# Performance work log

Measured on AMD Instinct MI355X. Metric: run time of the kernel, lower is better.

The kernel has to match this reference:

```python
import jax, jax.numpy as jnp
import numpy as np

BS = 4
EMBED = 256
HEADS = 8
LEVELS = 4
POINTS = 4
HD = EMBED // HEADS  # 32
SHAPES = np.array([[96, 96], [48, 48], [24, 24], [12, 12]], dtype=np.int64)
LQ = int((SHAPES[:, 0] * SHAPES[:, 1]).sum())  # 12240


def _offset_bias():
    # faithful to MSDeformableAttention._reset_parameters grid init
    thetas = np.arange(HEADS, dtype=np.float32) * (2.0 * np.pi / HEADS)
    g = np.stack([np.cos(thetas), np.sin(thetas)], -1)
    g = g / np.abs(g).max(-1, keepdims=True)
    g = np.tile(g.reshape(HEADS, 1, 1, 2), (1, LEVELS, POINTS, 1))
    g = g * np.arange(1, POINTS + 1, dtype=np.float32).reshape(1, 1, -1, 1)
    return jnp.asarray(g.reshape(-1), dtype=jnp.float32)


def setup_inputs() -> dict:
    key = jax.random.key(0)
    ks = jax.random.split(key, 8)
    tp = HEADS * LEVELS * POINTS
    d = {}
    d["query"] = jax.random.normal(ks[0], (BS, LQ, EMBED), jnp.float32)
    d["reference_points"] = jax.random.uniform(ks[1], (BS, LQ, LEVELS, 2), jnp.float32)
    d["value"] = jax.random.normal(ks[2], (BS, LQ, EMBED), jnp.float32)
    d["value_spatial_shapes"] = SHAPES  # static numpy, int
    d["W_off"] = jax.random.normal(ks[3], (EMBED, tp * 2), jnp.float32) * 0.01
    d["b_off"] = _offset_bias()
    d["W_attn"] = jax.random.normal(ks[4], (EMBED, tp), jnp.float32) * 0.02
    d["b_attn"] = jnp.zeros((tp,), jnp.float32)
    d["W_val"] = jax.random.normal(ks[5], (EMBED, EMBED), jnp.float32) * (1.0 / np.sqrt(EMBED).astype(np.float32))
    d["b_val"] = jnp.zeros((EMBED,), jnp.float32)
    d["W_out"] = jax.random.normal(ks[6], (EMBED, EMBED), jnp.float32) * (1.0 / np.sqrt(EMBED).astype(np.float32))
    d["b_out"] = jnp.zeros((EMBED,), jnp.float32)
    return d


def _bilinear_sample(img, grid):
    # img: [B,H,W,C]; grid: [B,Q,P,2] in [-1,1] (x,y)
    # matches F.grid_sample(mode='bilinear', padding_mode='zeros', align_corners=False)
    B, H, W, C = img.shape
    gx = (grid[..., 0] + 1.0) * (W * 0.5) - 0.5
    gy = (grid[..., 1] + 1.0) * (H * 0.5) - 0.5
    x0 = jnp.floor(gx)
    y0 = jnp.floor(gy)
    wx = gx - x0
    wy = gy - y0
    x0i = x0.astype(jnp.int32)
    y0i = y0.astype(jnp.int32)
    x1i = x0i + 1
    y1i = y0i + 1
    flat = img.reshape(B, H * W, C)

    def corner(xi, yi, w):
        valid = (xi >= 0) & (xi < W) & (yi >= 0) & (yi < H)
        idx = jnp.clip(yi, 0, H - 1) * W + jnp.clip(xi, 0, W - 1)
        v = jnp.take_along_axis(flat, idx.reshape(B, -1, 1), axis=1)
        v = v.reshape(idx.shape + (C,))
        return v * (w * valid)[..., None]

    return (corner(x0i, y0i, (1.0 - wx) * (1.0 - wy))
            + corner(x1i, y0i, wx * (1.0 - wy))
            + corner(x0i, y1i, (1.0 - wx) * wy)
            + corner(x1i, y1i, wx * wy))


def reference(query, reference_points, value, value_spatial_shapes,
              W_off, b_off, W_attn, b_attn, W_val, b_val, W_out, b_out):
    shapes = np.asarray(value_spatial_shapes)  # static [L,2] (H,W)
    bs, Lq, _ = query.shape
    v = (value @ W_val + b_val).reshape(bs, -1, HEADS, HD)  # [bs,Lv,H,hd]
    off = (query @ W_off + b_off).reshape(bs, Lq, HEADS, LEVELS, POINTS, 2)
    aw = jax.nn.softmax((query @ W_attn + b_attn).reshape(bs, Lq, HEADS, LEVELS * POINTS), axis=-1)
    aw = aw.reshape(bs, Lq, HEADS, LEVELS, POINTS)
    # normalizer is (W,H) per level
    norm = jnp.asarray(shapes[:, ::-1].copy(), jnp.float32).reshape(1, 1, 1, LEVELS, 1, 2)
    loc = reference_points[:, :, None, :, None, :] + off / norm
    grids = 2.0 * loc - 1.0  # [bs,Lq,H,L,P,2]

    acc = jnp.zeros((bs * HEADS, Lq, HD), query.dtype)
    start = 0
    for lvl in range(LEVELS):
        h, w = int(shapes[lvl, 0]), int(shapes[lvl, 1])
        v_l = v[:, start:start + h * w].reshape(bs, h, w, HEADS, HD)
        v_l = v_l.transpose(0, 3, 1, 2, 4).reshape(bs * HEADS, h, w, HD)
        g_l = grids[:, :, :, lvl].transpose(0, 2, 1, 3, 4).reshape(bs * HEADS, Lq, POINTS, 2)
        s_l = _bilinear_sample(v_l, g_l)  # [bs*H, Lq, P, hd]
        w_l = aw[:, :, :, lvl].transpose(0, 2, 1, 3).reshape(bs * HEADS, Lq, POINTS)
        acc = acc + jnp.einsum('bqpc,bqp->bqc', s_l, w_l)
        start += h * w

    out = acc.reshape(bs, HEADS, Lq, HD).transpose(0, 2, 1, 3).reshape(bs, Lq, EMBED)
    return out @ W_out + b_out
```

## Files before the change

kernel.cpp:

```cpp
#include <hip/hip_runtime.h>
#include <hip/hip_bf16.h>

static constexpr int BS     = 4;
static constexpr int EMBED  = 256;
static constexpr int HEADS  = 8;
static constexpr int LEVELS = 4;
static constexpr int POINTS = 4;
static constexpr int HD     = 32;
static constexpr int LQ     = 12240;
static constexpr int NROW   = BS * LQ;
static constexpr int LVL_W[4]  = {96, 48, 24, 12};
static constexpr int LVL_H[4]  = {96, 48, 24, 12};
static constexpr int LVL_ST[4] = {0, 9216, 11520, 12096};

typedef __attribute__((ext_vector_type(8))) short short8;
typedef __attribute__((ext_vector_type(4))) float f32x4;
typedef _Float16 h2 __attribute__((ext_vector_type(2)));

__device__ __forceinline__ unsigned short f2bf(float f) {
    unsigned int u = __float_as_uint(f);
    unsigned int r = (u + 0x7FFFu + ((u >> 16) & 1u)) >> 16;
    return (unsigned short)r;
}

__device__ __forceinline__ unsigned int pkh(float a, float b) {
    const unsigned int ua = __builtin_bit_cast(unsigned short, (_Float16)a);
    const unsigned int ub = __builtin_bit_cast(unsigned short, (_Float16)b);
    return ua | (ub << 16);
}

__device__ __forceinline__ float dot2(float acc, unsigned int v, unsigned int w) {
#if __has_builtin(__builtin_amdgcn_fdot2)
    return __builtin_amdgcn_fdot2(__builtin_bit_cast(h2, v),
                                  __builtin_bit_cast(h2, w), acc, false);
#else
    asm("v_dot2_f32_f16 %0, %1, %2, %0" : "+v"(acc) : "v"(v), "v"(w));
    return acc;
#endif
}

__global__ __launch_bounds__(256) void prep_weights(
    const float* __restrict__ W_off, const float* __restrict__ W_attn,
    const float* __restrict__ W_val, const float* __restrict__ W_out,
    unsigned short* __restrict__ WT_oa, unsigned short* __restrict__ WT_val,
    unsigned short* __restrict__ WT_out)
{
    const int gid = blockIdx.x * 256 + threadIdx.x;
    const int k = gid & 255;
    const int n = gid >> 8;
    if (n < 384) {
        const float v = (n < 256) ? W_off[k * 256 + n] : W_attn[k * 128 + (n - 256)];
        WT_oa[n * 256 + k] = f2bf(v);
    } else if (n < 640) {
        const int nn = n - 384;
        WT_val[nn * 256 + k] = f2bf(W_val[k * 256 + nn]);
    } else {
        const int nn = n - 640;
        WT_out[nn * 256 + k] = f2bf(W_out[k * 256 + nn]);
    }
}

template <int NCH, bool A_BF16, int OMODE>
__global__ __launch_bounds__(256, 3) void gemm_persist(
    const void* __restrict__ Av, const unsigned short* __restrict__ Wt,
    const float* __restrict__ bias0, const float* __restrict__ bias1, int nsplit,
    void* __restrict__ Cv)
{
    constexpr int K = 256;
    __shared__ __align__(16) unsigned short Af[64][264];
    __shared__ __align__(16) unsigned short Bs[128][40];

    const int tid = threadIdx.x;
    const int m0 = blockIdx.x * 64;
    const int w  = tid >> 6;
    const int l  = tid & 63;
    const int lm = l & 15;
    const int lq = l >> 4;

    const int sr = tid >> 2;
    const int kg = (tid & 3) * 8;

    if (A_BF16) {
        const unsigned short* A = (const unsigned short*)Av;
        #pragma unroll
        for (int k0 = 0; k0 < K; k0 += 32)
            *(short8*)&Af[sr][k0 + kg] = *(const short8*)&A[(size_t)(m0 + sr) * K + k0 + kg];
    } else {
        const float* A = (const float*)Av;
        #pragma unroll
        for (int k0 = 0; k0 < K; k0 += 32) {
            const float* ap = &A[(size_t)(m0 + sr) * K + k0 + kg];
            const float4 a0 = *(const float4*)ap;
            const float4 a1 = *(const float4*)(ap + 4);
            uint4 pk;
            pk.x = (unsigned int)f2bf(a0.x) | ((unsigned int)f2bf(a0.y) << 16);
            pk.y = (unsigned int)f2bf(a0.z) | ((unsigned int)f2bf(a0.w) << 16);
            pk.z = (unsigned int)f2bf(a1.x) | ((unsigned int)f2bf(a1.y) << 16);
            pk.w = (unsigned int)f2bf(a1.z) | ((unsigned int)f2bf(a1.w) << 16);
            *(uint4*)&Af[sr][k0 + kg] = pk;
        }
    }

    short8 pb[2];
    auto gloadB = [&](int n0, int k0) {
        #pragma unroll
        for (int i = 0; i < 2; ++i) {
            const int slot = tid + i * 256;
            const int n  = slot >> 2;
            const int kk = (slot & 3) * 8;
            pb[i] = *(const short8*)&Wt[(size_t)(n0 + n) * K + k0 + kk];
        }
    };
    gloadB(0, 0);
    __syncthreads();

    #pragma unroll
    for (int ch = 0; ch < NCH; ++ch) {
        const int n0 = ch * 128;
        f32x4 acc[4][2];
        #pragma unroll
        for (int rg = 0; rg < 4; ++rg) {
            acc[rg][0] = (f32x4){0.f, 0.f, 0.f, 0.f};
            acc[rg][1] = (f32x4){0.f, 0.f, 0.f, 0.f};
        }

        #pragma unroll 2
        for (int k0 = 0; k0 < K; k0 += 32) {
            #pragma unroll
            for (int i = 0; i < 2; ++i) {
                const int slot = tid + i * 256;
                const int n  = slot >> 2;
                const int kk = (slot & 3) * 8;
                *(short8*)&Bs[n][kk] = pb[i];
            }
            __syncthreads();

            if (k0 + 32 < K)       gloadB(n0, k0 + 32);
            else if (ch + 1 < NCH) gloadB(n0 + 128, 0);

            short8 af[4];
            #pragma unroll
            for (int rg = 0; rg < 4; ++rg)
                af[rg] = *(const short8*)&Af[rg * 16 + lm][k0 + lq * 8];
            #pragma unroll
            for (int nt = 0; nt < 2; ++nt) {
                const short8 bf = *(const short8*)&Bs[(w * 2 + nt) * 16 + lm][lq * 8];
                #pragma unroll
                for (int rg = 0; rg < 4; ++rg)
                    acc[rg][nt] = __builtin_amdgcn_mfma_f32_16x16x32_bf16(af[rg], bf, acc[rg][nt], 0, 0, 0);
            }
            __syncthreads();
        }

        #pragma unroll
        for (int nt = 0; nt < 2; ++nt) {
            const int col = n0 + (w * 2 + nt) * 16 + lm;
            const float b = (col < nsplit) ? bias0[col] : bias1[col - nsplit];
            #pragma unroll
            for (int rg = 0; rg < 4; ++rg)
                #pragma unroll
                for (int r = 0; r < 4; ++r) {
                    const int row = m0 + rg * 16 + lq * 4 + r;
                    const float v = acc[rg][nt][r] + b;
                    if (OMODE == 0)
                        ((unsigned short*)Cv)[(size_t)row * 256 + col] =
                            __builtin_bit_cast(unsigned short, (_Float16)v);
                    else if (OMODE == 1)
                        ((float*)Cv)[(size_t)row * 384 + col] = v;
                    else
                        ((float*)Cv)[(size_t)row * 256 + col] = v;
                }
        }
    }
}

__global__ __launch_bounds__(256, 4) void sample_kernel(
    const unsigned short* __restrict__ V,
    const float* __restrict__ OA,
    const float* __restrict__ refp,
    unsigned short* __restrict__ ACC)
{
    __shared__ __align__(16) unsigned int pr_o[512][4];
    __shared__ __align__(16) unsigned int pr_w[512][2];

    const int tid = threadIdx.x;

    const unsigned bx = blockIdx.x;
    const int xcd  = bx & 7;
    const int slot = bx >> 3;
    const int batch = xcd >> 1;
    const int wb   = slot * 2 + (xcd & 1);
    const int row0 = batch * LQ + wb * 4;

    {
        float4* dstb = (float4*)pr_o;
        const float4* src = (const float4*)(OA + (size_t)row0 * 384);
        {
            const int i = tid, rr = i / 96, ww = i % 96;
            dstb[rr * 96 + (ww ^ ((ww >> 3) & 7))] = src[i];
        }
        if (tid < 128) {
            const int i = tid + 256, rr = i / 96, ww = i % 96;
            dstb[rr * 96 + (ww ^ ((ww >> 3) & 7))] = src[i];
        }
        __syncthreads();

        const int g = tid & 31;
        const int r = g >> 3;
        const int h = g & 7;
        const int L = tid >> 5;
        const float* stg = (const float*)pr_o + r * 384;

        auto swzf4 = [](int f4) { return f4 ^ ((f4 >> 3) & 7); };

        const int f4l0 = 64 + ((h * 16 + L) >> 2);
        const int f4l1 = 64 + ((h * 16 + L + 8) >> 2);
        const float lg0 = stg[swzf4(f4l0) * 4 + (L & 3)];
        const float lg1 = stg[swzf4(f4l1) * 4 + (L & 3)];

        float* smax = (float*)pr_w;
        float* ssum = smax + 264;
        smax[L * 33 + g] = fmaxf(lg0, lg1);
        __syncthreads();
        float m = smax[g];
        #pragma unroll
        for (int k = 1; k < 8; ++k) m = fmaxf(m, smax[k * 33 + g]);
        const float e0 = __expf(lg0 - m);
        const float e1 = __expf(lg1 - m);
        ssum[L * 33 + g] = e0 + e1;
        __syncthreads();
        float sden = ssum[g];
        #pragma unroll
        for (int k = 1; k < 8; ++k) sden += ssum[k * 33 + g];
        const float inv = 1.0f / sden;

        uint4 ostash[2];
        uint2 wstash[2];
        int   sidx[2];
        #pragma unroll
        for (int ss = 0; ss < 2; ++ss) {
            const int lp  = L + ss * 8;
            const int s   = lp * 32 + g;
            const int lvl = lp >> 2;
            const int Wl = LVL_W[lvl], Hl = LVL_H[lvl], st = LVL_ST[lvl];

            const int f4c = h * 8 + (lp >> 1);
            const float2 oxy = *(const float2*)&stg[swzf4(f4c) * 4 + (lp & 1) * 2];
            const float2 rxy = *(const float2*)&refp[(size_t)(row0 + r) * 8 + lvl * 2];
            const float wgt = (ss ? e1 : e0) * inv;

            const float gx = (rxy.x + oxy.x / (float)Wl) * (float)Wl - 0.5f;
            const float gy = (rxy.y + oxy.y / (float)Hl) * (float)Hl - 0.5f;

            const float fx = floorf(gx), fy = floorf(gy);
            const float wx = gx - fx,    wy = gy - fy;
            const int x0 = (int)fx, y0 = (int)fy;
            const int x1 = x0 + 1,  y1 = y0 + 1;

            const bool bx0 = ((unsigned)x0 < (unsigned)Wl);
            const bool bx1 = ((unsigned)x1 < (unsigned)Wl);
            const bool by0 = ((unsigned)y0 < (unsigned)Hl);
            const bool by1 = ((unsigned)y1 < (unsigned)Hl);
            const float w00 = (bx0 && by0) ? (1.f - wx) * (1.f - wy) * wgt : 0.f;
            const float w10 = (bx1 && by0) ? wx * (1.f - wy) * wgt : 0.f;
            const float w01 = (bx0 && by1) ? (1.f - wx) * wy * wgt : 0.f;
            const float w11 = (bx1 && by1) ? wx * wy * wgt : 0.f;

            const int cx0 = min(max(x0, 0), Wl - 1);
            const int cx1 = min(max(x1, 0), Wl - 1);
            const int cy0 = min(max(y0, 0), Hl - 1);
            const int cy1 = min(max(y1, 0), Hl - 1);

            uint4 o;
            o.x = (unsigned int)(st + cy0 * Wl + cx0) * 512u;
            o.y = (unsigned int)(st + cy0 * Wl + cx1) * 512u;
            o.z = (unsigned int)(st + cy1 * Wl + cx0) * 512u;
            o.w = (unsigned int)(st + cy1 * Wl + cx1) * 512u;
            ostash[ss] = o;
            wstash[ss] = make_uint2(pkh(w00, w10), pkh(w01, w11));
            sidx[ss] = s;
        }
        __syncthreads();
        *(uint4*)&pr_o[sidx[0]][0] = ostash[0];
        *(uint4*)&pr_o[sidx[1]][0] = ostash[1];
        *(uint2*)&pr_w[sidx[0]][0] = wstash[0];
        *(uint2*)&pr_w[sidx[1]][0] = wstash[1];
    }
    __syncthreads();

    const int w    = tid >> 6;
    const int l    = tid & 63;
    const int half = l >> 5;
    const int head = (l >> 2) & 7;
    const int c16  = (l & 3) * 16;

    const int row  = __builtin_amdgcn_readfirstlane(row0 + w);
    const char* vrow = (const char*)V + (size_t)batch * ((size_t)LQ * 512);
    const unsigned int lane_byte = (unsigned int)(head * 64 + c16);
    const int sid0 = half * 256 + w * 8 + head;

    constexpr unsigned SEL_LO = 0x01000504u;
    constexpr unsigned SEL_HI = 0x03020706u;

    uint4 ofs[4];
    uint2 wpk[4];
    uint4 dat[3][4];
    float acc[8];
    #pragma unroll
    for (int i = 0; i < 8; ++i) acc[i] = 0.f;

    auto ldpr = [&](int j, int sl) {
        ofs[sl] = *(const uint4*)&pr_o[sid0 + j * 32][0];
        wpk[sl] = *(const uint2*)&pr_w[sid0 + j * 32][0];
    };
    auto ldglb = [&](int osl, int dsl) {
        const uint4 o = ofs[osl];
        dat[dsl][0] = *(const uint4*)(vrow + (lane_byte + o.x));
        dat[dsl][1] = *(const uint4*)(vrow + (lane_byte + o.y));
        dat[dsl][2] = *(const uint4*)(vrow + (lane_byte + o.z));
        dat[dsl][3] = *(const uint4*)(vrow + (lane_byte + o.w));
    };
    auto cpair = [&](const uint4& d0, const uint4& d1, unsigned wp) {
        acc[0] = dot2(acc[0], __builtin_amdgcn_perm(d0.x, d1.x, SEL_LO), wp);
        acc[1] = dot2(acc[1], __builtin_amdgcn_perm(d0.x, d1.x, SEL_HI), wp);
        acc[2] = dot2(acc[2], __builtin_amdgcn_perm(d0.y, d1.y, SEL_LO), wp);
        acc[3] = dot2(acc[3], __builtin_amdgcn_perm(d0.y, d1.y, SEL_HI), wp);
        acc[4] = dot2(acc[4], __builtin_amdgcn_perm(d0.z, d1.z, SEL_LO), wp);
        acc[5] = dot2(acc[5], __builtin_amdgcn_perm(d0.z, d1.z, SEL_HI), wp);
        acc[6] = dot2(acc[6], __builtin_amdgcn_perm(d0.w, d1.w, SEL_LO), wp);
        acc[7] = dot2(acc[7], __builtin_amdgcn_perm(d0.w, d1.w, SEL_HI), wp);
    };
    auto consume = [&](int dsl, int wsl) {
        cpair(dat[dsl][0], dat[dsl][1], wpk[wsl].x);
        cpair(dat[dsl][2], dat[dsl][3], wpk[wsl].y);
    };

    ldpr(0, 0); ldpr(1, 1); ldpr(2, 2);
    ldglb(0, 0); ldglb(1, 1);
    #pragma unroll
    for (int j = 0; j < 8; ++j) {
        if (j + 2 < 8) ldglb((j + 2) & 3, (j + 2) % 3);
        if (j + 3 < 8) ldpr(j + 3, (j + 3) & 3);
        consume(j % 3, j & 3);
    }

    #pragma unroll
    for (int i = 0; i < 8; ++i) acc[i] += __shfl_xor(acc[i], 32);

    if (half == 0) {
        uint4 o;
        o.x = (unsigned int)f2bf(acc[0]) | ((unsigned int)f2bf(acc[1]) << 16);
        o.y = (unsigned int)f2bf(acc[2]) | ((unsigned int)f2bf(acc[3]) << 16);
        o.z = (unsigned int)f2bf(acc[4]) | ((unsigned int)f2bf(acc[5]) << 16);
        o.w = (unsigned int)f2bf(acc[6]) | ((unsigned int)f2bf(acc[7]) << 16);
        *(uint4*)((char*)(ACC + (size_t)row * EMBED) + head * 64 + c16) = o;
    }
}

extern "C" void kernel_launch(void* const* d_in, const int* in_sizes, int n_in,
                              void* d_out, int out_size, void* d_ws, size_t ws_size,
                              hipStream_t stream) {
    const float* query  = (const float*)d_in[0];
    const float* refp   = (const float*)d_in[1];
    const float* value  = (const float*)d_in[2];
    const float* W_off  = (const float*)d_in[4];
    const float* b_off  = (const float*)d_in[5];
    const float* W_attn = (const float*)d_in[6];
    const float* b_attn = (const float*)d_in[7];
    const float* W_val  = (const float*)d_in[8];
    const float* b_val  = (const float*)d_in[9];
    const float* W_out  = (const float*)d_in[10];
    const float* b_out  = (const float*)d_in[11];
    float* out = (float*)d_out;

    unsigned short* WT_oa  = (unsigned short*)d_ws;
    unsigned short* WT_val = WT_oa  + 384 * 256;
    unsigned short* WT_out = WT_val + 256 * 256;
    unsigned short* V      = WT_out + 256 * 256;
    float*          OA     = (float*)(V + (size_t)NROW * EMBED);
    unsigned short* ACCb   = (unsigned short*)(OA + (size_t)NROW * 384);

    dim3 blk(256);

    prep_weights<<<896, blk, 0, stream>>>(W_off, W_attn, W_val, W_out,
                                          WT_oa, WT_val, WT_out);
    gemm_persist<2, false, 0><<<NROW / 64, blk, 0, stream>>>(
        value, WT_val, b_val, b_val, 256, V);
    gemm_persist<3, false, 1><<<NROW / 64, blk, 0, stream>>>(
        query, WT_oa, b_off, b_attn, 256, OA);
    sample_kernel<<<NROW / 4, blk, 0, stream>>>(V, OA, refp, ACCb);
    gemm_persist<2, true, 2><<<NROW / 64, blk, 0, stream>>>(
        ACCb, WT_out, b_out, b_out, 256, out);
}
```

Baseline: 320.1 us.

## Pre-convert inputs to bf16, use LDS-free direct-load GEMMs, tune sampler waits

A fused prep kernel now converts the weights and also the value and query activations to bf16 in one pass. The shared-memory-tiled GEMM is replaced by a direct-from-global MFMA GEMM over 32-row tiles, with no LDS or barriers. In the sampler, the LDS swizzle additionally XORs in the row index, and gathers use inline-asm loads with explicit vmcnt waits and sched barriers. Occupancy hints are relaxed. The trade-off is an extra activation round-trip through memory and more redundant global reads of A and W in the GEMMs.

```diff
diff --git a/kernel.cpp b/kernel.cpp
--- a/kernel.cpp
+++ b/kernel.cpp
@@ -39,117 +39,85 @@
 #endif
 }
 
-__global__ __launch_bounds__(256) void prep_weights(
+__global__ __launch_bounds__(256) void prep_all(
     const float* __restrict__ W_off, const float* __restrict__ W_attn,
     const float* __restrict__ W_val, const float* __restrict__ W_out,
+    const float* __restrict__ value, const float* __restrict__ query,
     unsigned short* __restrict__ WT_oa, unsigned short* __restrict__ WT_val,
-    unsigned short* __restrict__ WT_out)
+    unsigned short* __restrict__ WT_out,
+    unsigned short* __restrict__ Vb, unsigned short* __restrict__ Qb)
 {
-    const int gid = blockIdx.x * 256 + threadIdx.x;
-    const int k = gid & 255;
-    const int n = gid >> 8;
-    if (n < 384) {
-        const float v = (n < 256) ? W_off[k * 256 + n] : W_attn[k * 128 + (n - 256)];
-        WT_oa[n * 256 + k] = f2bf(v);
-    } else if (n < 640) {
-        const int nn = n - 384;
-        WT_val[nn * 256 + k] = f2bf(W_val[k * 256 + nn]);
-    } else {
-        const int nn = n - 640;
-        WT_out[nn * 256 + k] = f2bf(W_out[k * 256 + nn]);
-    }
-}
-
-template <int NCH, bool A_BF16, int OMODE>
-__global__ __launch_bounds__(256, 3) void gemm_persist(
-    const void* __restrict__ Av, const unsigned short* __restrict__ Wt,
+    const int bx = blockIdx.x;
+    const int tid = threadIdx.x;
+    if (bx < 896) {
+        const int gid = bx * 256 + tid;
+        const int k = gid & 255;
+        const int n = gid >> 8;
+        if (n < 384) {
+            const float v = (n < 256) ? W_off[k * 256 + n] : W_attn[k * 128 + (n - 256)];
+            WT_oa[n * 256 + k] = f2bf(v);
+        } else if (n < 640) {
+            const int nn = n - 384;
+            WT_val[nn * 256 + k] = f2bf(W_val[k * 256 + nn]);
+        } else {
+            const int nn = n - 640;
+            WT_out[nn * 256 + k] = f2bf(W_out[k * 256 + nn]);
+        }
+        return;
+    }
+    constexpr size_t NE = (size_t)NROW * 256;
+    const size_t i = ((size_t)(bx - 896) * 256 + tid) * 8;
+    const bool isV = (i < NE);
+    const float* src = isV ? value : query;
+    unsigned short* dst = isV ? Vb : Qb;
+    const size_t off = isV ? i : i - NE;
+    const float4 a0 = *(const float4*)&src[off];
+    const float4 a1 = *(const float4*)&src[off + 4];
+    uint4 pk;
+    pk.x = (unsigned int)f2bf(a0.x) | ((unsigned int)f2bf(a0.y) << 16);
+    pk.y = (unsigned int)f2bf(a0.z) | ((unsigned int)f2bf(a0.w) << 16);
+    pk.z = (unsigned int)f2bf(a1.x) | ((unsigned int)f2bf(a1.y) << 16);
+    pk.w = (unsigned int)f2bf(a1.z) | ((unsigned int)f2bf(a1.w) << 16);
+    *(uint4*)&dst[off] = pk;
+}
+
+template <int NCH, int OMODE>
+__global__ __launch_bounds__(256) void gemm_direct(
+    const unsigned short* __restrict__ A,
+    const unsigned short* __restrict__ Wt,
     const float* __restrict__ bias0, const float* __restrict__ bias1, int nsplit,
     void* __restrict__ Cv)
 {
-    constexpr int K = 256;
-    __shared__ __align__(16) unsigned short Af[64][264];
-    __shared__ __align__(16) unsigned short Bs[128][40];
-
     const int tid = threadIdx.x;
-    const int m0 = blockIdx.x * 64;
+    const int m0 = blockIdx.x * 32;
     const int w  = tid >> 6;
     const int l  = tid & 63;
     const int lm = l & 15;
     const int lq = l >> 4;
 
-    const int sr = tid >> 2;
-    const int kg = (tid & 3) * 8;
-
-    if (A_BF16) {
-        const unsigned short* A = (const unsigned short*)Av;
-        #pragma unroll
-        for (int k0 = 0; k0 < K; k0 += 32)
-            *(short8*)&Af[sr][k0 + kg] = *(const short8*)&A[(size_t)(m0 + sr) * K + k0 + kg];
-    } else {
-        const float* A = (const float*)Av;
-        #pragma unroll
-        for (int k0 = 0; k0 < K; k0 += 32) {
-            const float* ap = &A[(size_t)(m0 + sr) * K + k0 + kg];
-            const float4 a0 = *(const float4*)ap;
-            const float4 a1 = *(const float4*)(ap + 4);
-            uint4 pk;
-            pk.x = (unsigned int)f2bf(a0.x) | ((unsigned int)f2bf(a0.y) << 16);
-            pk.y = (unsigned int)f2bf(a0.z) | ((unsigned int)f2bf(a0.w) << 16);
-            pk.z = (unsigned int)f2bf(a1.x) | ((unsigned int)f2bf(a1.y) << 16);
-            pk.w = (unsigned int)f2bf(a1.z) | ((unsigned int)f2bf(a1.w) << 16);
-            *(uint4*)&Af[sr][k0 + kg] = pk;
-        }
-    }
-
-    short8 pb[2];
-    auto gloadB = [&](int n0, int k0) {
-        #pragma unroll
-        for (int i = 0; i < 2; ++i) {
-            const int slot = tid + i * 256;
-            const int n  = slot >> 2;
-            const int kk = (slot & 3) * 8;
-            pb[i] = *(const short8*)&Wt[(size_t)(n0 + n) * K + k0 + kk];
-        }
-    };
-    gloadB(0, 0);
-    __syncthreads();
+    const unsigned short* arow0 = &A[(size_t)(m0 + lm) * 256 + lq * 8];
+    const unsigned short* arow1 = arow0 + 16 * 256;
 
     #pragma unroll
     for (int ch = 0; ch < NCH; ++ch) {
         const int n0 = ch * 128;
-        f32x4 acc[4][2];
-        #pragma unroll
-        for (int rg = 0; rg < 4; ++rg) {
-            acc[rg][0] = (f32x4){0.f, 0.f, 0.f, 0.f};
-            acc[rg][1] = (f32x4){0.f, 0.f, 0.f, 0.f};
-        }
-
-        #pragma unroll 2
-        for (int k0 = 0; k0 < K; k0 += 32) {
-            #pragma unroll
-            for (int i = 0; i < 2; ++i) {
-                const int slot = tid + i * 256;
-                const int n  = slot >> 2;
-                const int kk = (slot & 3) * 8;
-                *(short8*)&Bs[n][kk] = pb[i];
-            }
-            __syncthreads();
-
-            if (k0 + 32 < K)       gloadB(n0, k0 + 32);
-            else if (ch + 1 < NCH) gloadB(n0 + 128, 0);
-
-            short8 af[4];
-            #pragma unroll
-            for (int rg = 0; rg < 4; ++rg)
-                af[rg] = *(const short8*)&Af[rg * 16 + lm][k0 + lq * 8];
-            #pragma unroll
-            for (int nt = 0; nt < 2; ++nt) {
-                const short8 bf = *(const short8*)&Bs[(w * 2 + nt) * 16 + lm][lq * 8];
-                #pragma unroll
-                for (int rg = 0; rg < 4; ++rg)
-                    acc[rg][nt] = __builtin_amdgcn_mfma_f32_16x16x32_bf16(af[rg], bf, acc[rg][nt], 0, 0, 0);
-            }
-            __syncthreads();
+        const unsigned short* b0 = &Wt[(size_t)(n0 + (w * 2) * 16 + lm) * 256 + lq * 8];
+        const unsigned short* b1 = b0 + 16 * 256;
+
+        f32x4 acc[2][2];
+        acc[0][0] = (f32x4){0.f,0.f,0.f,0.f}; acc[0][1] = (f32x4){0.f,0.f,0.f,0.f};
+        acc[1][0] = (f32x4){0.f,0.f,0.f,0.f}; acc[1][1] = (f32x4){0.f,0.f,0.f,0.f};
+
+        #pragma unroll
+        for (int k0 = 0; k0 < 256; k0 += 32) {
+            const short8 af0 = *(const short8*)(arow0 + k0);
+            const short8 af1 = *(const short8*)(arow1 + k0);
+            const short8 bf0 = *(const short8*)(b0 + k0);
+            const short8 bf1 = *(const short8*)(b1 + k0);
+            acc[0][0] = __builtin_amdgcn_mfma_f32_16x16x32_bf16(af0, bf0, acc[0][0], 0, 0, 0);
+            acc[1][0] = __builtin_amdgcn_mfma_f32_16x16x32_bf16(af1, bf0, acc[1][0], 0, 0, 0);
+            acc[0][1] = __builtin_amdgcn_mfma_f32_16x16x32_bf16(af0, bf1, acc[0][1], 0, 0, 0);
+            acc[1][1] = __builtin_amdgcn_mfma_f32_16x16x32_bf16(af1, bf1, acc[1][1], 0, 0, 0);
         }
 
         #pragma unroll
@@ -157,7 +125,7 @@
             const int col = n0 + (w * 2 + nt) * 16 + lm;
             const float b = (col < nsplit) ? bias0[col] : bias1[col - nsplit];
             #pragma unroll
-            for (int rg = 0; rg < 4; ++rg)
+            for (int rg = 0; rg < 2; ++rg)
                 #pragma unroll
                 for (int r = 0; r < 4; ++r) {
                     const int row = m0 + rg * 16 + lq * 4 + r;
@@ -174,7 +142,8 @@
     }
 }
 
-__global__ __launch_bounds__(256, 4) void sample_kernel(
+__global__ __launch_bounds__(256) __attribute__((amdgpu_waves_per_eu(3, 4)))
+void sample_kernel(
     const unsigned short* __restrict__ V,
     const float* __restrict__ OA,
     const float* __restrict__ refp,
@@ -197,11 +166,11 @@
         const float4* src = (const float4*)(OA + (size_t)row0 * 384);
         {
             const int i = tid, rr = i / 96, ww = i % 96;
-            dstb[rr * 96 + (ww ^ ((ww >> 3) & 7))] = src[i];
+            dstb[rr * 96 + (ww ^ ((ww >> 3) & 7) ^ rr)] = src[i];
         }
         if (tid < 128) {
             const int i = tid + 256, rr = i / 96, ww = i % 96;
-            dstb[rr * 96 + (ww ^ ((ww >> 3) & 7))] = src[i];
+            dstb[rr * 96 + (ww ^ ((ww >> 3) & 7) ^ rr)] = src[i];
         }
         __syncthreads();
 
@@ -211,7 +180,7 @@
         const int L = tid >> 5;
         const float* stg = (const float*)pr_o + r * 384;
 
-        auto swzf4 = [](int f4) { return f4 ^ ((f4 >> 3) & 7); };
+        auto swzf4 = [&](int f4) { return f4 ^ ((f4 >> 3) & 7) ^ r; };
 
         const int f4l0 = 64 + ((h * 16 + L) >> 2);
         const int f4l1 = 64 + ((h * 16 + L + 8) >> 2);
@@ -309,16 +278,19 @@
     #pragma unroll
     for (int i = 0; i < 8; ++i) acc[i] = 0.f;
 
+    auto gld = [](uint4& d, const char* p) {
+        asm volatile("global_load_dwordx4 %0, %1, off" : "=v"(d) : "v"(p));
+    };
     auto ldpr = [&](int j, int sl) {
         ofs[sl] = *(const uint4*)&pr_o[sid0 + j * 32][0];
         wpk[sl] = *(const uint2*)&pr_w[sid0 + j * 32][0];
     };
-    auto ldglb = [&](int osl, int dsl) {
-        const uint4 o = ofs[osl];
-        dat[dsl][0] = *(const uint4*)(vrow + (lane_byte + o.x));
-        dat[dsl][1] = *(const uint4*)(vrow + (lane_byte + o.y));
-        dat[dsl][2] = *(const uint4*)(vrow + (lane_byte + o.z));
-        dat[dsl][3] = *(const uint4*)(vrow + (lane_byte + o.w));
+    auto ldglb = [&](int j, int dsl) {
+        const uint4 o = ofs[j & 3];
+        gld(dat[dsl][0], vrow + (lane_byte + o.x));
+        gld(dat[dsl][1], vrow + (lane_byte + o.y));
+        gld(dat[dsl][2], vrow + (lane_byte + o.z));
+        gld(dat[dsl][3], vrow + (lane_byte + o.w));
     };
     auto cpair = [&](const uint4& d0, const uint4& d1, unsigned wp) {
         acc[0] = dot2(acc[0], __builtin_amdgcn_perm(d0.x, d1.x, SEL_LO), wp);
@@ -339,8 +311,12 @@
     ldglb(0, 0); ldglb(1, 1);
     #pragma unroll
     for (int j = 0; j < 8; ++j) {
-        if (j + 2 < 8) ldglb((j + 2) & 3, (j + 2) % 3);
+        if (j + 2 < 8) ldglb(j + 2, (j + 2) % 3);
         if (j + 3 < 8) ldpr(j + 3, (j + 3) & 3);
+        if (j <= 5)      asm volatile("s_waitcnt vmcnt(8)" ::: "memory");
+        else if (j == 6) asm volatile("s_waitcnt vmcnt(4)" ::: "memory");
+        else             asm volatile("s_waitcnt vmcnt(0)" ::: "memory");
+        __builtin_amdgcn_sched_barrier(0);
         consume(j % 3, j & 3);
     }
 
@@ -379,16 +355,15 @@
     unsigned short* V      = WT_out + 256 * 256;
     float*          OA     = (float*)(V + (size_t)NROW * EMBED);
     unsigned short* ACCb   = (unsigned short*)(OA + (size_t)NROW * 384);
+    unsigned short* Vb     = ACCb + (size_t)NROW * EMBED;
+    unsigned short* Qb     = ACCb;
 
     dim3 blk(256);
 
-    prep_weights<<<896, blk, 0, stream>>>(W_off, W_attn, W_val, W_out,
-                                          WT_oa, WT_val, WT_out);
-    gemm_persist<2, false, 0><<<NROW / 64, blk, 0, stream>>>(
-        value, WT_val, b_val, b_val, 256, V);
-    gemm_persist<3, false, 1><<<NROW / 64, blk, 0, stream>>>(
-        query, WT_oa, b_off, b_attn, 256, OA);
+    prep_all<<<13136, blk, 0, stream>>>(W_off, W_attn, W_val, W_out, value, query,
+                                        WT_oa, WT_val, WT_out, Vb, Qb);
+    gemm_direct<2, 0><<<1530, blk, 0, stream>>>(Vb, WT_val, b_val, b_val, 256, V);
+    gemm_direct<3, 1><<<1530, blk, 0, stream>>>(Qb, WT_oa, b_off, b_attn, 256, OA);
     sample_kernel<<<NROW / 4, blk, 0, stream>>>(V, OA, refp, ACCb);
-    gemm_persist<2, true, 2><<<NROW / 64, blk, 0, stream>>>(
-        ACCb, WT_out, b_out, b_out, 256, out);
-}
+    gemm_direct<2, 2><<<1530, blk, 0, stream>>>(ACCb, WT_out, b_out, b_out, 256, out);
+}
```

New measurement: 426.4 us. +33.2%, slower.
